# Kernel optimization log

Hardware: AMD Instinct MI355X
Metric: run time of the kernel (lower is better)

The kernel has to match this reference:

```python
import jax, jax.numpy as jnp
import numpy as np
from jax.ops import segment_sum

N = 100000


def _gcn_conv(h, W, b, row, col, dinv_row_col):
    # h: [N, d_in] -> [N, d_out]; PyG GCNConv: x@W, symmetric-normalized scatter-add, +bias
    h = h @ W
    msg = h[row] * dinv_row_col[:, None]          # [E+N, d_out]
    out = segment_sum(msg, col, num_segments=N)   # scatter-add to destination nodes
    return out + b


def setup_inputs() -> dict:
    key = jax.random.key(0)
    k1, k2, k3, k4, k5, k6 = jax.random.split(key, 6)
    E = 1200000
    x = jax.random.normal(k1, (N, 128), dtype=jnp.float32)
    edge_index = jax.random.randint(k2, (2, E), 0, N, dtype=jnp.int64)
    W1 = jax.random.normal(k3, (128, 64), dtype=jnp.float32) * (1.0 / np.sqrt(128))
    b1 = jax.random.normal(k4, (64,), dtype=jnp.float32) * 0.02
    W2 = jax.random.normal(k5, (64, 40), dtype=jnp.float32) * (1.0 / np.sqrt(64))
    b2 = jax.random.normal(k6, (40,), dtype=jnp.float32) * 0.02
    return {"x": x, "edge_index": edge_index, "W1": W1, "b1": b1, "W2": W2, "b2": b2}


def reference(x, edge_index, W1, b1, W2, b2):
    # Add self-loops (PyG GCNConv default add_self_loops=True)
    loop = jnp.arange(N, dtype=edge_index.dtype)
    row = jnp.concatenate([edge_index[0], loop])  # source
    col = jnp.concatenate([edge_index[1], loop])  # destination
    # Symmetric normalization: deg from destination (incl. self loops)
    deg = segment_sum(jnp.ones_like(col, dtype=x.dtype), col, num_segments=N)
    dinv = jnp.where(deg > 0, jax.lax.rsqrt(deg), 0.0)
    dinv_rc = dinv[row] * dinv[col]               # [E+N]

    hid = _gcn_conv(x, W1, b1, row, col, dinv_rc)
    hid = jax.nn.leaky_relu(hid, negative_slope=0.01)
    # dropout p=0 -> identity
    out = _gcn_conv(hid, W2, b2, row, col, dinv_rc)
    return out
```

## Files before the change

kernel.cpp:

```cpp
#include <hip/hip_runtime.h>

#define NN 100000
#define EE 1200000
#define NB 391
#define EPB 4096
#define BIN_BLK 293

typedef _Float16 half4 __attribute__((ext_vector_type(4)));
typedef _Float16 half8 __attribute__((ext_vector_type(8)));
typedef float    f32x4 __attribute__((ext_vector_type(4)));

__global__ __launch_bounds__(256) void k_zero_b(int* __restrict__ bcnt) {
  int i = blockIdx.x * 256 + threadIdx.x;
  if (i < NB) bcnt[i] = 0;
}

__global__ __launch_bounds__(256) void k_binhist(const int* __restrict__ col, int* __restrict__ bcnt) {
  __shared__ int lh[NB];
  int t = threadIdx.x;
  for (int i = t; i < NB; i += 256) lh[i] = 0;
  __syncthreads();
  int base = blockIdx.x * EPB;
  #pragma unroll
  for (int i = 0; i < 16; ++i) {
    int e = base + i * 256 + t;
    if (e < EE) atomicAdd(&lh[col[e] >> 8], 1);
  }
  __syncthreads();
  for (int i = t; i < NB; i += 256) {
    int v = lh[i];
    if (v) atomicAdd(&bcnt[i], v);
  }
}

__global__ __launch_bounds__(512) void k_binscan(const int* __restrict__ bcnt, int* __restrict__ bptr,
                                                 int* __restrict__ bcur, int* __restrict__ row_ptr) {
  __shared__ int sm[512];
  int t = threadIdx.x;
  int v = (t < NB) ? bcnt[t] : 0;
  sm[t] = v;
  __syncthreads();
  for (int off = 1; off < 512; off <<= 1) {
    int u = (t >= off) ? sm[t - off] : 0;
    __syncthreads();
    sm[t] += u;
    __syncthreads();
  }
  int excl = sm[t] - v;
  if (t < NB) { bptr[t] = excl; bcur[t] = excl; }
  if (t == 0) { bptr[NB] = EE; row_ptr[NN] = EE; }
}

__global__ __launch_bounds__(256) void k_binfill(const int* __restrict__ row, const int* __restrict__ col,
                                                 int* __restrict__ bcur, int* __restrict__ binned) {
  __shared__ int lh[NB];
  __shared__ int lbase[NB];
  int t = threadIdx.x;
  for (int i = t; i < NB; i += 256) lh[i] = 0;
  __syncthreads();
  int base = blockIdx.x * EPB;
  #pragma unroll
  for (int i = 0; i < 16; ++i) {
    int e = base + i * 256 + t;
    if (e < EE) atomicAdd(&lh[col[e] >> 8], 1);
  }
  __syncthreads();
  for (int i = t; i < NB; i += 256) {
    int v = lh[i];
    lbase[i] = v ? atomicAdd(&bcur[i], v) : 0;
  }
  __syncthreads();
  for (int i = t; i < NB; i += 256) lh[i] = 0;
  __syncthreads();
  #pragma unroll
  for (int i = 0; i < 16; ++i) {
    int e = base + i * 256 + t;
    if (e < EE) {
      int c = col[e];
      int b = c >> 8;
      int p = lbase[b] + atomicAdd(&lh[b], 1);
      binned[p] = (row[e] << 8) | (c & 255);
    }
  }
}

__global__ __launch_bounds__(256) void k_build2(const int* __restrict__ binned, const int* __restrict__ bptr,
                                                int* __restrict__ row_ptr, int* __restrict__ src,
                                                float* __restrict__ dinv) {
  __shared__ int cnt[256];
  __shared__ int sm[256];
  __shared__ int cur[256];
  int t = threadIdx.x;
  int b = blockIdx.x;
  int nb0 = b << 8;
  int nnode = NN - nb0 < 256 ? NN - nb0 : 256;
  int ebeg = bptr[b], eend = bptr[b + 1];
  cnt[t] = 0;
  __syncthreads();
  for (int e = ebeg + t; e < eend; e += 256)
    atomicAdd(&cnt[binned[e] & 255], 1);
  __syncthreads();
  int v = cnt[t];
  sm[t] = v;
  __syncthreads();
  for (int off = 1; off < 256; off <<= 1) {
    int u = (t >= off) ? sm[t - off] : 0;
    __syncthreads();
    sm[t] += u;
    __syncthreads();
  }
  int excl = sm[t] - v;
  if (t < nnode) {
    row_ptr[nb0 + t] = ebeg + excl;
    dinv[nb0 + t] = rsqrtf((float)v + 1.0f);
  }
  cur[t] = excl;
  __syncthreads();
  for (int e = ebeg + t; e < eend; e += 256) {
    int rc = binned[e];
    int cl = rc & 255;
    int p = ebeg + atomicAdd(&cur[cl], 1);
    src[p] = rc >> 8;
  }
}

__global__ __launch_bounds__(256) void k_gemm1(const float* __restrict__ x, const float* __restrict__ W,
                                               const float* __restrict__ dinv, _Float16* __restrict__ g) {
  __shared__ _Float16 xh[64 * 136];
  __shared__ _Float16 Wt[64 * 136];
  const int t = threadIdx.x;
  const int row0 = blockIdx.x * 64;

  #pragma unroll
  for (int p = 0; p < 8; ++p) {
    int idx = t + p * 256;
    int k = idx >> 4;
    int n4 = (idx & 15) << 2;
    float4 v = *reinterpret_cast<const float4*>(&W[k * 64 + n4]);
    Wt[(n4 + 0) * 136 + k] = (_Float16)v.x;
    Wt[(n4 + 1) * 136 + k] = (_Float16)v.y;
    Wt[(n4 + 2) * 136 + k] = (_Float16)v.z;
    Wt[(n4 + 3) * 136 + k] = (_Float16)v.w;
  }
  #pragma unroll
  for (int p = 0; p < 4; ++p) {
    int idx = t + p * 256;
    int r = idx >> 4;
    int k8 = idx & 15;
    int grow = row0 + r;
    half8 h = {0, 0, 0, 0, 0, 0, 0, 0};
    if (grow < NN) {
      float4 a0 = *reinterpret_cast<const float4*>(&x[(size_t)grow * 128 + k8 * 8]);
      float4 a1 = *reinterpret_cast<const float4*>(&x[(size_t)grow * 128 + k8 * 8 + 4]);
      h[0] = (_Float16)a0.x; h[1] = (_Float16)a0.y; h[2] = (_Float16)a0.z; h[3] = (_Float16)a0.w;
      h[4] = (_Float16)a1.x; h[5] = (_Float16)a1.y; h[6] = (_Float16)a1.z; h[7] = (_Float16)a1.w;
    }
    *reinterpret_cast<half8*>(&xh[r * 136 + k8 * 8]) = h;
  }
  __syncthreads();

  const int w = t >> 6;
  const int l = t & 63;
  const int lrow = l & 15;
  const int kg = l >> 4;

  f32x4 z = {0.0f, 0.0f, 0.0f, 0.0f};
  f32x4 acc[4];
  acc[0] = z; acc[1] = z; acc[2] = z; acc[3] = z;

  const _Float16* xb = &xh[(w * 16 + lrow) * 136 + kg * 8];
  #pragma unroll
  for (int s = 0; s < 4; ++s) {
    half8 a = *reinterpret_cast<const half8*>(xb + s * 32);
    #pragma unroll
    for (int nt = 0; nt < 4; ++nt) {
      half8 b = *reinterpret_cast<const half8*>(&Wt[(nt * 16 + lrow) * 136 + kg * 8 + s * 32]);
      acc[nt] = __builtin_amdgcn_mfma_f32_16x16x32_f16(a, b, acc[nt], 0, 0, 0);
    }
  }

  float dv[4];
  #pragma unroll
  for (int r = 0; r < 4; ++r) {
    int grow = row0 + w * 16 + kg * 4 + r;
    dv[r] = (grow < NN) ? dinv[grow] : 0.0f;
  }
  #pragma unroll
  for (int nt = 0; nt < 4; ++nt)
    #pragma unroll
    for (int r = 0; r < 4; ++r) {
      int grow = row0 + w * 16 + kg * 4 + r;
      if (grow < NN)
        g[(size_t)grow * 64 + nt * 16 + lrow] = (_Float16)(acc[nt][r] * dv[r]);
    }
}

__global__ __launch_bounds__(256) void k_gather1(const int* __restrict__ row_ptr, const int* __restrict__ src,
                                                 const _Float16* __restrict__ g, const float* __restrict__ dinv,
                                                 const float* __restrict__ b1, _Float16* __restrict__ hid) {
  int t = threadIdx.x;
  int node = blockIdx.x * 16 + (t >> 4);
  if (node >= NN) return;
  int q = (t & 15) << 2;
  int beg = row_ptr[node], end = row_ptr[node + 1];
  half4 sv = *reinterpret_cast<const half4*>(&g[(size_t)node * 64 + q]);
  float4 acc = make_float4((float)sv.x, (float)sv.y, (float)sv.z, (float)sv.w);
  int e = beg;
  for (; e + 3 < end; e += 4) {
    int s0 = src[e], s1 = src[e + 1], s2 = src[e + 2], s3 = src[e + 3];
    half4 v0 = *reinterpret_cast<const half4*>(&g[(size_t)s0 * 64 + q]);
    half4 v1 = *reinterpret_cast<const half4*>(&g[(size_t)s1 * 64 + q]);
    half4 v2 = *reinterpret_cast<const half4*>(&g[(size_t)s2 * 64 + q]);
    half4 v3 = *reinterpret_cast<const half4*>(&g[(size_t)s3 * 64 + q]);
    acc.x += ((float)v0.x + (float)v1.x) + ((float)v2.x + (float)v3.x);
    acc.y += ((float)v0.y + (float)v1.y) + ((float)v2.y + (float)v3.y);
    acc.z += ((float)v0.z + (float)v1.z) + ((float)v2.z + (float)v3.z);
    acc.w += ((float)v0.w + (float)v1.w) + ((float)v2.w + (float)v3.w);
  }
  for (; e < end; ++e) {
    int s0 = src[e];
    half4 v0 = *reinterpret_cast<const half4*>(&g[(size_t)s0 * 64 + q]);
    acc.x += (float)v0.x; acc.y += (float)v0.y; acc.z += (float)v0.z; acc.w += (float)v0.w;
  }
  float dv = dinv[node];
  float4 bv = *reinterpret_cast<const float4*>(&b1[q]);
  float4 o;
  o.x = acc.x * dv + bv.x; o.y = acc.y * dv + bv.y;
  o.z = acc.z * dv + bv.z; o.w = acc.w * dv + bv.w;
  o.x = o.x > 0.f ? o.x : 0.01f * o.x;
  o.y = o.y > 0.f ? o.y : 0.01f * o.y;
  o.z = o.z > 0.f ? o.z : 0.01f * o.z;
  o.w = o.w > 0.f ? o.w : 0.01f * o.w;
  half4 ho;
  ho.x = (_Float16)o.x; ho.y = (_Float16)o.y; ho.z = (_Float16)o.z; ho.w = (_Float16)o.w;
  *reinterpret_cast<half4*>(&hid[(size_t)node * 64 + q]) = ho;
}

__global__ __launch_bounds__(256) void k_gemm2(const _Float16* __restrict__ hid, const float* __restrict__ W,
                                               const float* __restrict__ dinv, _Float16* __restrict__ g2) {
  __shared__ _Float16 xh[64 * 72];
  __shared__ _Float16 Wt[48 * 72];
  const int t = threadIdx.x;
  const int row0 = blockIdx.x * 64;

  #pragma unroll
  for (int p = 0; p < 12; ++p) {
    int idx = t + p * 256;
    int n = idx >> 6, k = idx & 63;
    _Float16 v = (_Float16)0.0f;
    if (n < 40) v = (_Float16)W[k * 40 + n];
    Wt[n * 72 + k] = v;
  }
  #pragma unroll
  for (int p = 0; p < 2; ++p) {
    int idx = t + p * 256;
    int r = idx >> 3, k8 = idx & 7;
    int grow = row0 + r;
    half8 h = {0, 0, 0, 0, 0, 0, 0, 0};
    if (grow < NN) h = *reinterpret_cast<const half8*>(&hid[(size_t)grow * 64 + k8 * 8]);
    *reinterpret_cast<half8*>(&xh[r * 72 + k8 * 8]) = h;
  }
  __syncthreads();

  const int w = t >> 6;
  const int l = t & 63;
  const int lrow = l & 15;
  const int kg = l >> 4;

  f32x4 z = {0.0f, 0.0f, 0.0f, 0.0f};
  f32x4 acc[3];
  acc[0] = z; acc[1] = z; acc[2] = z;

  const _Float16* xb = &xh[(w * 16 + lrow) * 72 + kg * 8];
  #pragma unroll
  for (int s = 0; s < 2; ++s) {
    half8 a = *reinterpret_cast<const half8*>(xb + s * 32);
    #pragma unroll
    for (int nt = 0; nt < 3; ++nt) {
      half8 b = *reinterpret_cast<const half8*>(&Wt[(nt * 16 + lrow) * 72 + kg * 8 + s * 32]);
      acc[nt] = __builtin_amdgcn_mfma_f32_16x16x32_f16(a, b, acc[nt], 0, 0, 0);
    }
  }

  float dv[4];
  #pragma unroll
  for (int r = 0; r < 4; ++r) {
    int grow = row0 + w * 16 + kg * 4 + r;
    dv[r] = (grow < NN) ? dinv[grow] : 0.0f;
  }
  #pragma unroll
  for (int nt = 0; nt < 3; ++nt) {
    int colv = nt * 16 + lrow;
    #pragma unroll
    for (int r = 0; r < 4; ++r) {
      int grow = row0 + w * 16 + kg * 4 + r;
      if (grow < NN && colv < 40)
        g2[(size_t)grow * 40 + colv] = (_Float16)(acc[nt][r] * dv[r]);
    }
  }
}

__global__ __launch_bounds__(320) void k_gather2(const int* __restrict__ row_ptr, const int* __restrict__ src,
                                                 const _Float16* __restrict__ g2, const float* __restrict__ dinv,
                                                 const float* __restrict__ b2, float* __restrict__ out) {
  int t = threadIdx.x;
  int local = t / 10;
  int grp = t - local * 10;
  int node = blockIdx.x * 32 + local;
  if (node >= NN) return;
  int q = grp * 4;
  int beg = row_ptr[node], end = row_ptr[node + 1];
  half4 sv = *reinterpret_cast<const half4*>(&g2[(size_t)node * 40 + q]);
  float4 acc = make_float4((float)sv.x, (float)sv.y, (float)sv.z, (float)sv.w);
  int e = beg;
  for (; e + 3 < end; e += 4) {
    int s0 = src[e], s1 = src[e + 1], s2 = src[e + 2], s3 = src[e + 3];
    half4 v0 = *reinterpret_cast<const half4*>(&g2[(size_t)s0 * 40 + q]);
    half4 v1 = *reinterpret_cast<const half4*>(&g2[(size_t)s1 * 40 + q]);
    half4 v2 = *reinterpret_cast<const half4*>(&g2[(size_t)s2 * 40 + q]);
    half4 v3 = *reinterpret_cast<const half4*>(&g2[(size_t)s3 * 40 + q]);
    acc.x += ((float)v0.x + (float)v1.x) + ((float)v2.x + (float)v3.x);
    acc.y += ((float)v0.y + (float)v1.y) + ((float)v2.y + (float)v3.y);
    acc.z += ((float)v0.z + (float)v1.z) + ((float)v2.z + (float)v3.z);
    acc.w += ((float)v0.w + (float)v1.w) + ((float)v2.w + (float)v3.w);
  }
  for (; e < end; ++e) {
    int s0 = src[e];
    half4 v0 = *reinterpret_cast<const half4*>(&g2[(size_t)s0 * 40 + q]);
    acc.x += (float)v0.x; acc.y += (float)v0.y; acc.z += (float)v0.z; acc.w += (float)v0.w;
  }
  float dv = dinv[node];
  float4 bv = *reinterpret_cast<const float4*>(&b2[q]);
  float4 o;
  o.x = acc.x * dv + bv.x; o.y = acc.y * dv + bv.y;
  o.z = acc.z * dv + bv.z; o.w = acc.w * dv + bv.w;
  *reinterpret_cast<float4*>(&out[(size_t)node * 40 + q]) = o;
}

extern "C" void kernel_launch(void* const* d_in, const int* in_sizes, int n_in,
                              void* d_out, int out_size, void* d_ws, size_t ws_size,
                              hipStream_t stream) {
  const float* x  = (const float*)d_in[0];
  const int*   ei = (const int*)d_in[1];
  const float* W1 = (const float*)d_in[2];
  const float* b1 = (const float*)d_in[3];
  const float* W2 = (const float*)d_in[4];
  const float* b2 = (const float*)d_in[5];
  float* out = (float*)d_out;

  const int* row = ei;
  const int* col = ei + EE;

  float* ws      = (float*)d_ws;
  float* dinv    = ws;
  int*   row_ptr = (int*)(ws + 100352);
  int*   bptr    = row_ptr + 100352;
  int*   bcnt    = bptr + 512;
  int*   bcur    = bcnt + 512;
  int*   src     = bcur + 512;
  _Float16* g1   = (_Float16*)(src + 1200128);
  _Float16* hid  = (_Float16*)((char*)g1 + 12800000);
  _Float16* g2   = g1;
  int*   binned  = (int*)g1;

  k_zero_b <<<2, 256, 0, stream>>>(bcnt);
  k_binhist<<<BIN_BLK, 256, 0, stream>>>(col, bcnt);
  k_binscan<<<1, 512, 0, stream>>>(bcnt, bptr, bcur, row_ptr);
  k_binfill<<<BIN_BLK, 256, 0, stream>>>(row, col, bcur, binned);
  k_build2 <<<NB, 256, 0, stream>>>(binned, bptr, row_ptr, src, dinv);

  k_gemm1  <<<(NN + 63) / 64, 256, 0, stream>>>(x, W1, dinv, g1);
  k_gather1<<<(NN + 15) / 16, 256, 0, stream>>>(row_ptr, src, g1, dinv, b1, hid);

  k_gemm2  <<<(NN + 63) / 64, 256, 0, stream>>>(hid, W2, dinv, g2);
  k_gather2<<<(NN + 31) / 32, 320, 0, stream>>>(row_ptr, src, g2, dinv, b2, out);
}
```

Baseline: 228.3 us.

## Fuse layer-1 gather with layer-2 GEMM and replace zero kernel with memset

The first-layer gather now keeps its leaky-ReLU output in shared memory and multiplies it by W2 there using scalar FMAs. It then writes the dinv-scaled g2 directly, which removes the separate k_gemm2 launch and the round trip of the hid buffer through global memory. Every block now loads the full W2 (10 KB) into LDS and runs the small GEMM on CUDA-style FP32 FMAs instead of MFMA. This adds LDS traffic and a barrier to the memory-bound gather. The tiny zeroing kernel is replaced by hipMemsetAsync.

After: 232.1 us. Within noise of the previous version (+1.7%).

```diff
diff --git a/kernel.cpp b/kernel.cpp
--- a/kernel.cpp
+++ b/kernel.cpp
@@ -9,11 +9,6 @@
 typedef _Float16 half4 __attribute__((ext_vector_type(4)));
 typedef _Float16 half8 __attribute__((ext_vector_type(8)));
 typedef float    f32x4 __attribute__((ext_vector_type(4)));
-
-__global__ __launch_bounds__(256) void k_zero_b(int* __restrict__ bcnt) {
-  int i = blockIdx.x * 256 + threadIdx.x;
-  if (i < NB) bcnt[i] = 0;
-}
 
 __global__ __launch_bounds__(256) void k_binhist(const int* __restrict__ col, int* __restrict__ bcnt) {
   __shared__ int lh[NB];
@@ -195,108 +190,81 @@
     }
 }
 
-__global__ __launch_bounds__(256) void k_gather1(const int* __restrict__ row_ptr, const int* __restrict__ src,
-                                                 const _Float16* __restrict__ g, const float* __restrict__ dinv,
-                                                 const float* __restrict__ b1, _Float16* __restrict__ hid) {
-  int t = threadIdx.x;
-  int node = blockIdx.x * 16 + (t >> 4);
-  if (node >= NN) return;
+__global__ __launch_bounds__(256) void k_gather1f(const int* __restrict__ row_ptr, const int* __restrict__ src,
+                                                  const _Float16* __restrict__ g, const float* __restrict__ dinv,
+                                                  const float* __restrict__ b1, const float* __restrict__ W2,
+                                                  _Float16* __restrict__ g2) {
+  __shared__ float hidS[16 * 68];
+  __shared__ float Ws2[2576];
+  int t = threadIdx.x;
+  if (t < 16) Ws2[2560 + t] = 0.0f;
+  for (int i = t; i < 640; i += 256)
+    *reinterpret_cast<float4*>(&Ws2[i * 4]) = *reinterpret_cast<const float4*>(&W2[i * 4]);
+
+  int nl = t >> 4;
+  int node = blockIdx.x * 16 + nl;
   int q = (t & 15) << 2;
-  int beg = row_ptr[node], end = row_ptr[node + 1];
-  half4 sv = *reinterpret_cast<const half4*>(&g[(size_t)node * 64 + q]);
-  float4 acc = make_float4((float)sv.x, (float)sv.y, (float)sv.z, (float)sv.w);
-  int e = beg;
-  for (; e + 3 < end; e += 4) {
-    int s0 = src[e], s1 = src[e + 1], s2 = src[e + 2], s3 = src[e + 3];
-    half4 v0 = *reinterpret_cast<const half4*>(&g[(size_t)s0 * 64 + q]);
-    half4 v1 = *reinterpret_cast<const half4*>(&g[(size_t)s1 * 64 + q]);
-    half4 v2 = *reinterpret_cast<const half4*>(&g[(size_t)s2 * 64 + q]);
-    half4 v3 = *reinterpret_cast<const half4*>(&g[(size_t)s3 * 64 + q]);
-    acc.x += ((float)v0.x + (float)v1.x) + ((float)v2.x + (float)v3.x);
-    acc.y += ((float)v0.y + (float)v1.y) + ((float)v2.y + (float)v3.y);
-    acc.z += ((float)v0.z + (float)v1.z) + ((float)v2.z + (float)v3.z);
-    acc.w += ((float)v0.w + (float)v1.w) + ((float)v2.w + (float)v3.w);
-  }
-  for (; e < end; ++e) {
-    int s0 = src[e];
-    half4 v0 = *reinterpret_cast<const half4*>(&g[(size_t)s0 * 64 + q]);
-    acc.x += (float)v0.x; acc.y += (float)v0.y; acc.z += (float)v0.z; acc.w += (float)v0.w;
-  }
-  float dv = dinv[node];
-  float4 bv = *reinterpret_cast<const float4*>(&b1[q]);
-  float4 o;
-  o.x = acc.x * dv + bv.x; o.y = acc.y * dv + bv.y;
-  o.z = acc.z * dv + bv.z; o.w = acc.w * dv + bv.w;
-  o.x = o.x > 0.f ? o.x : 0.01f * o.x;
-  o.y = o.y > 0.f ? o.y : 0.01f * o.y;
-  o.z = o.z > 0.f ? o.z : 0.01f * o.z;
-  o.w = o.w > 0.f ? o.w : 0.01f * o.w;
-  half4 ho;
-  ho.x = (_Float16)o.x; ho.y = (_Float16)o.y; ho.z = (_Float16)o.z; ho.w = (_Float16)o.w;
-  *reinterpret_cast<half4*>(&hid[(size_t)node * 64 + q]) = ho;
-}
-
-__global__ __launch_bounds__(256) void k_gemm2(const _Float16* __restrict__ hid, const float* __restrict__ W,
-                                               const float* __restrict__ dinv, _Float16* __restrict__ g2) {
-  __shared__ _Float16 xh[64 * 72];
-  __shared__ _Float16 Wt[48 * 72];
-  const int t = threadIdx.x;
-  const int row0 = blockIdx.x * 64;
-
-  #pragma unroll
-  for (int p = 0; p < 12; ++p) {
-    int idx = t + p * 256;
-    int n = idx >> 6, k = idx & 63;
-    _Float16 v = (_Float16)0.0f;
-    if (n < 40) v = (_Float16)W[k * 40 + n];
-    Wt[n * 72 + k] = v;
-  }
-  #pragma unroll
-  for (int p = 0; p < 2; ++p) {
-    int idx = t + p * 256;
-    int r = idx >> 3, k8 = idx & 7;
-    int grow = row0 + r;
-    half8 h = {0, 0, 0, 0, 0, 0, 0, 0};
-    if (grow < NN) h = *reinterpret_cast<const half8*>(&hid[(size_t)grow * 64 + k8 * 8]);
-    *reinterpret_cast<half8*>(&xh[r * 72 + k8 * 8]) = h;
-  }
-  __syncthreads();
-
-  const int w = t >> 6;
-  const int l = t & 63;
-  const int lrow = l & 15;
-  const int kg = l >> 4;
-
-  f32x4 z = {0.0f, 0.0f, 0.0f, 0.0f};
-  f32x4 acc[3];
-  acc[0] = z; acc[1] = z; acc[2] = z;
-
-  const _Float16* xb = &xh[(w * 16 + lrow) * 72 + kg * 8];
-  #pragma unroll
-  for (int s = 0; s < 2; ++s) {
-    half8 a = *reinterpret_cast<const half8*>(xb + s * 32);
-    #pragma unroll
-    for (int nt = 0; nt < 3; ++nt) {
-      half8 b = *reinterpret_cast<const half8*>(&Wt[(nt * 16 + lrow) * 72 + kg * 8 + s * 32]);
-      acc[nt] = __builtin_amdgcn_mfma_f32_16x16x32_f16(a, b, acc[nt], 0, 0, 0);
-    }
-  }
-
-  float dv[4];
-  #pragma unroll
-  for (int r = 0; r < 4; ++r) {
-    int grow = row0 + w * 16 + kg * 4 + r;
-    dv[r] = (grow < NN) ? dinv[grow] : 0.0f;
-  }
-  #pragma unroll
-  for (int nt = 0; nt < 3; ++nt) {
-    int colv = nt * 16 + lrow;
-    #pragma unroll
-    for (int r = 0; r < 4; ++r) {
-      int grow = row0 + w * 16 + kg * 4 + r;
-      if (grow < NN && colv < 40)
-        g2[(size_t)grow * 40 + colv] = (_Float16)(acc[nt][r] * dv[r]);
-    }
+  bool valid = node < NN;
+  float dvv = 0.0f;
+  float4 o = make_float4(0.f, 0.f, 0.f, 0.f);
+  if (valid) {
+    int beg = row_ptr[node], end = row_ptr[node + 1];
+    half4 sv = *reinterpret_cast<const half4*>(&g[(size_t)node * 64 + q]);
+    float4 acc = make_float4((float)sv.x, (float)sv.y, (float)sv.z, (float)sv.w);
+    int e = beg;
+    for (; e + 3 < end; e += 4) {
+      int s0 = src[e], s1 = src[e + 1], s2 = src[e + 2], s3 = src[e + 3];
+      half4 v0 = *reinterpret_cast<const half4*>(&g[(size_t)s0 * 64 + q]);
+      half4 v1 = *reinterpret_cast<const half4*>(&g[(size_t)s1 * 64 + q]);
+      half4 v2 = *reinterpret_cast<const half4*>(&g[(size_t)s2 * 64 + q]);
+      half4 v3 = *reinterpret_cast<const half4*>(&g[(size_t)s3 * 64 + q]);
+      acc.x += ((float)v0.x + (float)v1.x) + ((float)v2.x + (float)v3.x);
+      acc.y += ((float)v0.y + (float)v1.y) + ((float)v2.y + (float)v3.y);
+      acc.z += ((float)v0.z + (float)v1.z) + ((float)v2.z + (float)v3.z);
+      acc.w += ((float)v0.w + (float)v1.w) + ((float)v2.w + (float)v3.w);
+    }
+    for (; e < end; ++e) {
+      int s0 = src[e];
+      half4 v0 = *reinterpret_cast<const half4*>(&g[(size_t)s0 * 64 + q]);
+      acc.x += (float)v0.x; acc.y += (float)v0.y; acc.z += (float)v0.z; acc.w += (float)v0.w;
+    }
+    dvv = dinv[node];
+    float4 bv = *reinterpret_cast<const float4*>(&b1[q]);
+    o.x = acc.x * dvv + bv.x; o.y = acc.y * dvv + bv.y;
+    o.z = acc.z * dvv + bv.z; o.w = acc.w * dvv + bv.w;
+    o.x = o.x > 0.f ? o.x : 0.01f * o.x;
+    o.y = o.y > 0.f ? o.y : 0.01f * o.y;
+    o.z = o.z > 0.f ? o.z : 0.01f * o.z;
+    o.w = o.w > 0.f ? o.w : 0.01f * o.w;
+  }
+  *reinterpret_cast<float4*>(&hidS[nl * 68 + q]) = o;
+  __syncthreads();
+
+  int j = t & 15;
+  float a0 = 0.f, a1 = 0.f, a2 = 0.f;
+  const float* hrow = &hidS[nl * 68];
+  #pragma unroll
+  for (int k4 = 0; k4 < 16; ++k4) {
+    float4 hv = *reinterpret_cast<const float4*>(&hrow[k4 * 4]);
+    int kb = k4 * 4 * 40 + j;
+    a0 = fmaf(hv.x, Ws2[kb + 0 * 40],      a0);
+    a1 = fmaf(hv.x, Ws2[kb + 0 * 40 + 16], a1);
+    a2 = fmaf(hv.x, Ws2[kb + 0 * 40 + 32], a2);
+    a0 = fmaf(hv.y, Ws2[kb + 1 * 40],      a0);
+    a1 = fmaf(hv.y, Ws2[kb + 1 * 40 + 16], a1);
+    a2 = fmaf(hv.y, Ws2[kb + 1 * 40 + 32], a2);
+    a0 = fmaf(hv.z, Ws2[kb + 2 * 40],      a0);
+    a1 = fmaf(hv.z, Ws2[kb + 2 * 40 + 16], a1);
+    a2 = fmaf(hv.z, Ws2[kb + 2 * 40 + 32], a2);
+    a0 = fmaf(hv.w, Ws2[kb + 3 * 40],      a0);
+    a1 = fmaf(hv.w, Ws2[kb + 3 * 40 + 16], a1);
+    a2 = fmaf(hv.w, Ws2[kb + 3 * 40 + 32], a2);
+  }
+  if (valid) {
+    g2[(size_t)node * 40 + j]      = (_Float16)(a0 * dvv);
+    g2[(size_t)node * 40 + j + 16] = (_Float16)(a1 * dvv);
+    if (j < 8)
+      g2[(size_t)node * 40 + j + 32] = (_Float16)(a2 * dvv);
   }
 }
 
@@ -359,19 +327,16 @@
   int*   bcur    = bcnt + 512;
   int*   src     = bcur + 512;
   _Float16* g1   = (_Float16*)(src + 1200128);
-  _Float16* hid  = (_Float16*)((char*)g1 + 12800000);
-  _Float16* g2   = g1;
+  _Float16* g2   = (_Float16*)((char*)g1 + 12800000);
   int*   binned  = (int*)g1;
 
-  k_zero_b <<<2, 256, 0, stream>>>(bcnt);
+  hipMemsetAsync(bcnt, 0, 512 * sizeof(int), stream);
   k_binhist<<<BIN_BLK, 256, 0, stream>>>(col, bcnt);
   k_binscan<<<1, 512, 0, stream>>>(bcnt, bptr, bcur, row_ptr);
   k_binfill<<<BIN_BLK, 256, 0, stream>>>(row, col, bcur, binned);
   k_build2 <<<NB, 256, 0, stream>>>(binned, bptr, row_ptr, src, dinv);
 
   k_gemm1  <<<(NN + 63) / 64, 256, 0, stream>>>(x, W1, dinv, g1);
-  k_gather1<<<(NN + 15) / 16, 256, 0, stream>>>(row_ptr, src, g1, dinv, b1, hid);
-
-  k_gemm2  <<<(NN + 63) / 64, 256, 0, stream>>>(hid, W2, dinv, g2);
+  k_gather1f<<<(NN + 15) / 16, 256, 0, stream>>>(row_ptr, src, g1, dinv, b1, W2, g2);
   k_gather2<<<(NN + 31) / 32, 320, 0, stream>>>(row_ptr, src, g2, dinv, b2, out);
 }
```
